# Kernel optimization log

Hardware: AMD Instinct MI355X
Metric: run time of the kernel (lower is better)

The kernel has to match this reference:

```python
import jax, jax.numpy as jnp
import numpy as np

N_NODES = 100000
N_EDGES = 1600000
D = 64
N_RELS = 200
LEAKY_SLOPE = 0.01


def setup_inputs() -> dict:
    key = jax.random.key(0)
    ks = jax.random.split(key, 12)
    def xavier(k, shape):
        gain = float(np.sqrt(2.0))  # calculate_gain('relu')
        bound = gain * float(np.sqrt(6.0 / (shape[0] + shape[1])))
        return jax.random.uniform(k, shape, jnp.float32, -bound, bound)
    return {
        "h": jax.random.normal(ks[0], (N_NODES, D), jnp.float32),
        "rel_emb": jax.random.normal(ks[1], (N_RELS, D), jnp.float32),
        "weight_neighbor": xavier(ks[2], (2 * D, D)),
        "attn_w": (xavier(ks[3], (3 * D, 1))).reshape(3 * D),
        "delta": jnp.ones((1,), jnp.float32),
        "loop_weight": xavier(ks[4], (D, D)),
        "evolve_loop_weight": xavier(ks[5], (D, D)),
        "etime": jax.random.uniform(ks[6], (N_EDGES,), jnp.float32),
        "src": jax.random.randint(ks[7], (N_EDGES,), 0, N_NODES),
        "dst": jax.random.randint(ks[8], (N_EDGES,), 0, N_NODES),
        "etype": jax.random.randint(ks[9], (N_EDGES,), 0, N_RELS),
    }


def reference(h, rel_emb, weight_neighbor, attn_w, delta, loop_weight,
              evolve_loop_weight, etime, src, dst, etype):
    N, d = h.shape
    # cat(src_h, rel) @ W  ==  src_h @ W[:d] + rel @ W[d:]  (precompute per node / per relation)
    hW = h @ weight_neighbor[:d]                 # [N, d]
    relW = rel_emb @ weight_neighbor[d:]         # [R, d]
    # attn_fc(cat(src_h, dst_h, rel)) == per-node/per-rel scalar contributions
    a1, a2, a3 = attn_w[:d], attn_w[d:2 * d], attn_w[2 * d:]
    s_src = h @ a1                               # [N]
    s_dst = h @ a2                               # [N]
    s_rel = rel_emb @ a3                         # [R]
    e = jax.nn.leaky_relu(s_src[src] + s_dst[dst] + s_rel[etype], LEAKY_SLOPE)  # [E]
    k = -etime * delta[0]                        # [E]
    scores = k * e                               # [E]
    # segment softmax over in-edges of each destination node
    m = jax.ops.segment_max(scores, dst, num_segments=N)          # [N]
    ex = jnp.exp(scores - m[dst])                                  # [E]
    den = jax.ops.segment_sum(ex, dst, num_segments=N)             # [N]
    w = ex / den[dst]                                              # [E]
    msg = hW[src] + relW[etype]                                    # [E, d]
    agg = jax.ops.segment_sum(w[:, None] * msg, dst, num_segments=N)  # [N, d]
    # nodes with no in-edges keep original h (DGL update_all semantics)
    deg = jax.ops.segment_sum(jnp.ones_like(scores), dst, num_segments=N)
    has_in = (deg > 0)[:, None]
    loop = jnp.where(has_in, h @ loop_weight, h @ evolve_loop_weight)
    node_repr = jnp.where(has_in, agg, h) + loop
    return node_repr
```

## Files before the change

kernel.cpp:

```cpp
#include <hip/hip_runtime.h>
#include <hip/hip_bf16.h>

#define N_NODES 100000
#define N_EDGES 1600000
#define D       64
#define N_RELS  200
#define LEAKY   0.01f
#define NBUCK   ((N_NODES + 511) / 512)
#define BIN_CHUNK 4096
#define NBIN    ((N_EDGES + BIN_CHUNK - 1) / BIN_CHUNK)

typedef __hip_bfloat16 bf16;

__device__ __forceinline__ float b2f(bf16 x) { return __bfloat162float(x); }
__device__ __forceinline__ bf16  f2b(float x) { return __float2bfloat16(x); }

__device__ __forceinline__ float ldf(const void* p, long i, int bf) {
    return bf ? __bfloat162float(((const bf16*)p)[i]) : ((const float*)p)[i];
}
__device__ __forceinline__ int probe_bf(const void* delta) {
    return ((const unsigned short*)delta)[0] == 0x3F80 ? 1 : 0;
}

__device__ __forceinline__ int rl_i(int v, int l) {
    return __builtin_amdgcn_readlane(v, l);
}
__device__ __forceinline__ float rl_f(float v, int l) {
    return __int_as_float(__builtin_amdgcn_readlane(__float_as_int(v), l));
}

__global__ __launch_bounds__(512, 4) void k_fused_proj(const void* __restrict__ h,
                                                       const void* __restrict__ wn,
                                                       const void* __restrict__ attn,
                                                       const void* __restrict__ delta,
                                                       const void* __restrict__ rel_emb,
                                                       const int* __restrict__ dst,
                                                       bf16* __restrict__ hWb,
                                                       float* __restrict__ s_src,
                                                       float* __restrict__ s_dst,
                                                       float* __restrict__ relW,
                                                       float* __restrict__ s_rel,
                                                       int* __restrict__ bcnt) {
    __shared__ int bh[NBUCK];
    const int bf = probe_bf(delta);
    const int wave = threadIdx.x >> 6;
    const int lane = threadIdx.x & 63;
    const int gw = blockIdx.x * 8 + wave;
    const int nwaves = gridDim.x * 8;
    float wreg[D];
    #pragma unroll
    for (int k = 0; k < D; k++) wreg[k] = ldf(wn, (long)k * D + lane, bf);
    const float a1 = ldf(attn, lane, bf);
    const float a2 = ldf(attn, D + lane, bf);
    for (int base = gw * 4; base < N_NODES; base += nwaves * 4) {
        float hv[4], acc[4];
        #pragma unroll
        for (int j = 0; j < 4; j++) {
            hv[j] = ldf(h, (long)(base + j) * D + lane, bf);
            acc[j] = 0.f;
        }
        #pragma unroll
        for (int j = 0; j < 4; j++) {
            float p1 = hv[j] * a1, p2 = hv[j] * a2;
            #pragma unroll
            for (int off = 32; off; off >>= 1) { p1 += __shfl_xor(p1, off); p2 += __shfl_xor(p2, off); }
            if (lane == 0) { s_src[base + j] = p1; s_dst[base + j] = p2; }
        }
        #pragma unroll
        for (int k = 0; k < D; k++) {
            float w = wreg[k];
            acc[0] += rl_f(hv[0], k) * w;
            acc[1] += rl_f(hv[1], k) * w;
            acc[2] += rl_f(hv[2], k) * w;
            acc[3] += rl_f(hv[3], k) * w;
        }
        #pragma unroll
        for (int j = 0; j < 4; j++) hWb[(long)(base + j) * D + lane] = f2b(acc[j]);
    }
    const float a3 = ldf(attn, 2 * D + lane, bf);
    for (int r = gw; r < N_RELS; r += nwaves) {
        float rv = ldf(rel_emb, (long)r * D + lane, bf);
        float p3 = rv * a3;
        #pragma unroll
        for (int off = 32; off; off >>= 1) p3 += __shfl_xor(p3, off);
        if (lane == 0) s_rel[r] = p3;
        float acc = 0.f;
        #pragma unroll
        for (int k = 0; k < D; k++) {
            acc += rl_f(rv, k) * ldf(wn, (long)(D + k) * D + lane, bf);
        }
        relW[r * D + lane] = acc;
    }
    for (int t = threadIdx.x; t < NBUCK; t += 512) bh[t] = 0;
    __syncthreads();
    for (int t = blockIdx.x * 512 + threadIdx.x; t < N_EDGES; t += gridDim.x * 512)
        atomicAdd(&bh[dst[t] >> 9], 1);
    __syncthreads();
    for (int t = threadIdx.x; t < NBUCK; t += 512) {
        int v = bh[t];
        if (v) atomicAdd(&bcnt[t], v);
    }
}

__global__ __launch_bounds__(256) void k_bscan(const int* __restrict__ bcnt,
                                               int* __restrict__ bbase,
                                               int* __restrict__ bcursor,
                                               int* __restrict__ rowptr) {
    __shared__ int s[256];
    const int tid = threadIdx.x;
    int v = (tid < NBUCK) ? bcnt[tid] : 0;
    s[tid] = v;
    __syncthreads();
    for (int off = 1; off < 256; off <<= 1) {
        int t = (tid >= off) ? s[tid - off] : 0;
        __syncthreads();
        s[tid] += t;
        __syncthreads();
    }
    if (tid < NBUCK) {
        int e = s[tid] - v;
        bbase[tid] = e;
        bcursor[tid] = e;
    }
    if (tid == 255) {
        bbase[NBUCK] = s[255];
        rowptr[N_NODES] = s[255];
    }
}

__global__ __launch_bounds__(512, 2) void k_bin(const float* __restrict__ s_src,
                                                const float* __restrict__ s_dst,
                                                const float* __restrict__ s_rel,
                                                const void* __restrict__ etime,
                                                const void* __restrict__ delta,
                                                const int* __restrict__ src,
                                                const int* __restrict__ dst,
                                                const int* __restrict__ etype,
                                                int* __restrict__ bcursor,
                                                int4* __restrict__ binned) {
    __shared__ int lh[NBUCK];
    __shared__ int lbase[NBUCK];
    __shared__ int gbase[NBUCK];
    __shared__ int sc[256];
    __shared__ int4 stage[BIN_CHUNK];
    const int bf = probe_bf(delta);
    const float df = ldf(delta, 0, bf);
    const int tid = threadIdx.x;
    const int base = blockIdx.x * BIN_CHUNK;
    for (int t = tid; t < NBUCK; t += 512) lh[t] = 0;
    __syncthreads();
    int4 rc[8];
    int rk[8], bk[8];
    #pragma unroll
    for (int j = 0; j < 8; j++) {
        int e = base + j * 512 + tid;
        bk[j] = -1;
        if (e < N_EDGES) {
            int s = src[e], d = dst[e], r = etype[e];
            float scv = s_src[s] + s_dst[d] + s_rel[r];
            float lre = scv > 0.f ? scv : LEAKY * scv;
            float score = (-ldf(etime, e, bf) * df) * lre;
            rc[j].x = __float_as_int(__expf(score));
            rc[j].y = s | (r << 17);
            rc[j].z = d & 511;
            rc[j].w = 0;
            int b = d >> 9;
            bk[j] = b;
            rk[j] = atomicAdd(&lh[b], 1);
        }
    }
    __syncthreads();
    if (tid < 256) sc[tid] = (tid < NBUCK) ? lh[tid] : 0;
    __syncthreads();
    for (int off = 1; off < 256; off <<= 1) {
        int t = 0;
        if (tid < 256 && tid >= off) t = sc[tid - off];
        __syncthreads();
        if (tid < 256) sc[tid] += t;
        __syncthreads();
    }
    if (tid < NBUCK) {
        lbase[tid] = sc[tid] - lh[tid];
        if (lh[tid] > 0) gbase[tid] = atomicAdd(&bcursor[tid], lh[tid]);
    }
    __syncthreads();
    #pragma unroll
    for (int j = 0; j < 8; j++) {
        if (bk[j] >= 0) stage[lbase[bk[j]] + rk[j]] = rc[j];
    }
    __syncthreads();
    const int wave = tid >> 6, lane = tid & 63;
    for (int b = wave; b < NBUCK; b += 8) {
        int n = lh[b];
        if (!n) continue;
        int ls = lbase[b];
        int gd = gbase[b];
        for (int k = lane; k < n; k += 64) binned[gd + k] = stage[ls + k];
    }
}

__global__ __launch_bounds__(1024) void k_bucket(const int4* __restrict__ binned,
                                                 const int* __restrict__ bbase,
                                                 int* __restrict__ rowptr,
                                                 int2* __restrict__ sorted) {
    __shared__ int fh[512];
    __shared__ int fc[512];
    __shared__ int sc[512];
    const int tid = threadIdx.x;
    const int b = blockIdx.x;
    const int n0 = b << 9;
    const int s0 = bbase[b], s1 = bbase[b + 1];
    if (tid < 512) { fh[tid] = 0; fc[tid] = 0; }
    __syncthreads();
    for (int i = s0 + tid; i < s1; i += 1024) atomicAdd(&fh[binned[i].z], 1);
    __syncthreads();
    if (tid < 512) sc[tid] = fh[tid];
    __syncthreads();
    for (int off = 1; off < 512; off <<= 1) {
        int t = 0;
        if (tid < 512 && tid >= off) t = sc[tid - off];
        __syncthreads();
        if (tid < 512) sc[tid] += t;
        __syncthreads();
    }
    int excl = 0;
    if (tid < 512) excl = sc[tid] - fh[tid];
    __syncthreads();
    if (tid < 512) {
        fh[tid] = excl;
        if (n0 + tid < N_NODES) rowptr[n0 + tid] = s0 + excl;
    }
    __syncthreads();
    for (int i = s0 + tid; i < s1; i += 1024) {
        int4 r = binned[i];
        int p = s0 + fh[r.z] + atomicAdd(&fc[r.z], 1);
        sorted[p] = make_int2(r.x, r.y);
    }
}

__global__ __launch_bounds__(512, 4) void k_loop(const void* __restrict__ h,
                                                 const void* __restrict__ loopW,
                                                 const void* __restrict__ delta,
                                                 float* __restrict__ L) {
    const int bf = probe_bf(delta);
    const int wave = threadIdx.x >> 6;
    const int lane = threadIdx.x & 63;
    const int gw = blockIdx.x * 8 + wave;
    const int nwaves = gridDim.x * 8;
    float wreg[D];
    #pragma unroll
    for (int k = 0; k < D; k++) wreg[k] = ldf(loopW, (long)k * D + lane, bf);
    for (int base = gw * 4; base < N_NODES; base += nwaves * 4) {
        float hv[4], acc[4];
        #pragma unroll
        for (int j = 0; j < 4; j++) {
            hv[j] = ldf(h, (long)(base + j) * D + lane, bf);
            acc[j] = 0.f;
        }
        #pragma unroll
        for (int k = 0; k < D; k++) {
            float w = wreg[k];
            acc[0] += rl_f(hv[0], k) * w;
            acc[1] += rl_f(hv[1], k) * w;
            acc[2] += rl_f(hv[2], k) * w;
            acc[3] += rl_f(hv[3], k) * w;
        }
        #pragma unroll
        for (int j = 0; j < 4; j++) L[(long)(base + j) * D + lane] = acc[j];
    }
}

__global__ __launch_bounds__(512, 8) void k_aggregate(const int* __restrict__ rowptr,
                                                      const int2* __restrict__ sorted,
                                                      const bf16* __restrict__ hWb,
                                                      const float* __restrict__ relW,
                                                      const void* __restrict__ h,
                                                      const void* __restrict__ evolveW,
                                                      const float* __restrict__ L,
                                                      const void* __restrict__ delta,
                                                      float* __restrict__ out) {
    const int bf = probe_bf(delta);
    const int wave = threadIdx.x >> 6;
    const int lane = threadIdx.x & 63;
    const int grp  = lane >> 4;
    const int sub  = lane & 15;
    const unsigned sub8  = (unsigned)sub << 3;
    const unsigned sub16 = (unsigned)sub << 4;
    const int wstride = gridDim.x * 8;
    for (int i = blockIdx.x * 8 + wave; i < N_NODES; i += wstride) {
        const int s0 = rowptr[i], e1 = rowptr[i + 1];
        if (e1 > s0) {
            float ax = 0.f, ay = 0.f, az = 0.f, aw = 0.f;
            float ls = 0.f;
            for (int c = s0; c < e1; c += 64) {
                int n = e1 - c; n = n > 64 ? 64 : n;
                float exl = 0.f; int pk = 0;
                if (lane < n) {
                    int2 rec = sorted[c + lane];
                    exl = __int_as_float(rec.x);
                    pk = rec.y;
                }
                float cs = exl;
                #pragma unroll
                for (int off = 32; off; off >>= 1) cs += __shfl_xor(cs, off);
                ls += cs;
                #pragma unroll 2
                for (int j = 0; j < n; j += 4) {
                    float w = __shfl(exl, j + grp);
                    int   p = __shfl(pk,  j + grp);
                    unsigned hoff = ((unsigned)(p & 0x1FFFF) << 7) + sub8;
                    unsigned roff = ((unsigned)(p >> 17) << 8) + sub16;
                    uint2  hw = *(const uint2*) ((const char*)hWb  + hoff);
                    float4 rw = *(const float4*)((const char*)relW + roff);
                    float f0 = __uint_as_float(hw.x << 16);
                    float f1 = __uint_as_float(hw.x & 0xFFFF0000u);
                    float f2 = __uint_as_float(hw.y << 16);
                    float f3 = __uint_as_float(hw.y & 0xFFFF0000u);
                    ax += w * (f0 + rw.x);
                    ay += w * (f1 + rw.y);
                    az += w * (f2 + rw.z);
                    aw += w * (f3 + rw.w);
                }
            }
            ax += __shfl_xor(ax, 16); ax += __shfl_xor(ax, 32);
            ay += __shfl_xor(ay, 16); ay += __shfl_xor(ay, 32);
            az += __shfl_xor(az, 16); az += __shfl_xor(az, 32);
            aw += __shfl_xor(aw, 16); aw += __shfl_xor(aw, 32);
            if (grp == 0) {
                const float inv = 1.f / ls;
                const float4 l4 = *(const float4*)(L + (long)i * D + sub * 4);
                float4 r;
                r.x = ax * inv + l4.x;
                r.y = ay * inv + l4.y;
                r.z = az * inv + l4.z;
                r.w = aw * inv + l4.w;
                *(float4*)(out + (long)i * D + sub * 4) = r;
            }
        } else {
            float hv = ldf(h, (long)i * D + lane, bf);
            float acc = hv;
            for (int k = 0; k < D; k++)
                acc += rl_f(hv, k) * ldf(evolveW, (long)k * D + lane, bf);
            out[(long)i * D + lane] = acc;
        }
    }
}

__global__ __launch_bounds__(256) void k_fallback(float* __restrict__ out) {
    int t = blockIdx.x * blockDim.x + threadIdx.x;
    if (t < N_NODES * D) out[t] = 0.f;
}

extern "C" void kernel_launch(void* const* d_in, const int* in_sizes, int n_in,
                              void* d_out, int out_size, void* d_ws, size_t ws_size,
                              hipStream_t stream) {
    const void* h       = d_in[0];
    const void* rel_emb = d_in[1];
    const void* wn      = d_in[2];
    const void* attn    = d_in[3];
    const void* delta   = d_in[4];
    const void* loopW   = d_in[5];
    const void* evolveW = d_in[6];
    const void* etime   = d_in[7];
    const int*  src     = (const int*)d_in[8];
    const int*  dst     = (const int*)d_in[9];
    const int*  etype   = (const int*)d_in[10];
    float* out = (float*)d_out;

    char* ws = (char*)d_ws;
    size_t off = 0;
    auto alloc = [&](size_t bytes) -> void* {
        off = (off + 255) & ~(size_t)255;
        void* p = ws + off;
        off += bytes;
        return p;
    };
    int4*  binned  = (int4*) alloc((size_t)N_EDGES * 16);
    int2*  sorted  = (int2*) alloc((size_t)N_EDGES * 8);
    bf16*  hWb     = (bf16*) alloc((size_t)N_NODES * D * 2);
    float* relW    = (float*)alloc((size_t)N_RELS * D * 4);
    float* s_src   = (float*)alloc((size_t)N_NODES * 4);
    float* s_dst   = (float*)alloc((size_t)N_NODES * 4);
    float* s_rel   = (float*)alloc((size_t)N_RELS * 4);
    int*   rowptr  = (int*)  alloc((size_t)(N_NODES + 1) * 4);
    int*   bcnt    = (int*)  alloc((size_t)NBUCK * 4);
    int*   bbase   = (int*)  alloc((size_t)(NBUCK + 1) * 4);
    int*   bcursor = (int*)  alloc((size_t)NBUCK * 4);

    float* L = (float*)binned;

    if (ws_size < off) {
        k_fallback<<<(N_NODES * D + 255) / 256, 256, 0, stream>>>(out);
        return;
    }

    hipMemsetAsync(bcnt, 0, (size_t)NBUCK * 4, stream);
    k_fused_proj<<<1024, 512, 0, stream>>>(h, wn, attn, delta, rel_emb, dst,
                                           hWb, s_src, s_dst, relW, s_rel, bcnt);
    k_bscan<<<1, 256, 0, stream>>>(bcnt, bbase, bcursor, rowptr);
    k_bin<<<NBIN, 512, 0, stream>>>(s_src, s_dst, s_rel, etime, delta,
                                    src, dst, etype, bcursor, binned);
    k_bucket<<<NBUCK, 1024, 0, stream>>>(binned, bbase, rowptr, sorted);
    k_loop<<<1024, 512, 0, stream>>>(h, loopW, delta, L);
    k_aggregate<<<2048, 512, 0, stream>>>(rowptr, sorted, hWb, relW, h, evolveW, L, delta, out);
}
```

Measured before the change: 309.7 us.

## Shrink binned edge records, use finer buckets, drop LDS staging in binning

The binned edge record drops from 16 bytes to an 8-byte payload plus a separate byte-sized local index, and buckets shrink from 512 to 256 nodes, so the bucket sort handles smaller groups. k_bin no longer stages records in shared memory and instead scatters directly to global positions, which removes an LDS scan and a copy pass but makes the writes less coalesced. The projection kernel now processes 8 nodes per wave instead of 4, runs with a smaller grid, and only 256 blocks build the histogram. Launch bounds are raised to 8 blocks per CU, which may cause register spills in the 64-register weight loops.

```diff
diff --git a/kernel.cpp b/kernel.cpp
--- a/kernel.cpp
+++ b/kernel.cpp
@@ -6,9 +6,11 @@
 #define D       64
 #define N_RELS  200
 #define LEAKY   0.01f
-#define NBUCK   ((N_NODES + 511) / 512)
-#define BIN_CHUNK 4096
-#define NBIN    ((N_EDGES + BIN_CHUNK - 1) / BIN_CHUNK)
+#define NBUCK      391
+#define BUCK_SHIFT 8
+#define BUCK_MASK  255
+#define BIN_CHUNK  4096
+#define NBIN       ((N_EDGES + BIN_CHUNK - 1) / BIN_CHUNK)
 
 typedef __hip_bfloat16 bf16;
 
@@ -29,7 +31,7 @@
     return __int_as_float(__builtin_amdgcn_readlane(__float_as_int(v), l));
 }
 
-__global__ __launch_bounds__(512, 4) void k_fused_proj(const void* __restrict__ h,
+__global__ __launch_bounds__(512, 8) void k_fused_proj(const void* __restrict__ h,
                                                        const void* __restrict__ wn,
                                                        const void* __restrict__ attn,
                                                        const void* __restrict__ delta,
@@ -52,15 +54,15 @@
     for (int k = 0; k < D; k++) wreg[k] = ldf(wn, (long)k * D + lane, bf);
     const float a1 = ldf(attn, lane, bf);
     const float a2 = ldf(attn, D + lane, bf);
-    for (int base = gw * 4; base < N_NODES; base += nwaves * 4) {
-        float hv[4], acc[4];
-        #pragma unroll
-        for (int j = 0; j < 4; j++) {
+    for (int base = gw * 8; base < N_NODES; base += nwaves * 8) {
+        float hv[8], acc[8];
+        #pragma unroll
+        for (int j = 0; j < 8; j++) {
             hv[j] = ldf(h, (long)(base + j) * D + lane, bf);
             acc[j] = 0.f;
         }
         #pragma unroll
-        for (int j = 0; j < 4; j++) {
+        for (int j = 0; j < 8; j++) {
             float p1 = hv[j] * a1, p2 = hv[j] * a2;
             #pragma unroll
             for (int off = 32; off; off >>= 1) { p1 += __shfl_xor(p1, off); p2 += __shfl_xor(p2, off); }
@@ -69,13 +71,11 @@
         #pragma unroll
         for (int k = 0; k < D; k++) {
             float w = wreg[k];
-            acc[0] += rl_f(hv[0], k) * w;
-            acc[1] += rl_f(hv[1], k) * w;
-            acc[2] += rl_f(hv[2], k) * w;
-            acc[3] += rl_f(hv[3], k) * w;
-        }
-        #pragma unroll
-        for (int j = 0; j < 4; j++) hWb[(long)(base + j) * D + lane] = f2b(acc[j]);
+            #pragma unroll
+            for (int j = 0; j < 8; j++) acc[j] += rl_f(hv[j], k) * w;
+        }
+        #pragma unroll
+        for (int j = 0; j < 8; j++) hWb[(long)(base + j) * D + lane] = f2b(acc[j]);
     }
     const float a3 = ldf(attn, 2 * D + lane, bf);
     for (int r = gw; r < N_RELS; r += nwaves) {
@@ -91,27 +91,29 @@
         }
         relW[r * D + lane] = acc;
     }
-    for (int t = threadIdx.x; t < NBUCK; t += 512) bh[t] = 0;
-    __syncthreads();
-    for (int t = blockIdx.x * 512 + threadIdx.x; t < N_EDGES; t += gridDim.x * 512)
-        atomicAdd(&bh[dst[t] >> 9], 1);
-    __syncthreads();
-    for (int t = threadIdx.x; t < NBUCK; t += 512) {
-        int v = bh[t];
-        if (v) atomicAdd(&bcnt[t], v);
-    }
-}
-
-__global__ __launch_bounds__(256) void k_bscan(const int* __restrict__ bcnt,
+    if (blockIdx.x < 256) {
+        for (int t = threadIdx.x; t < NBUCK; t += 512) bh[t] = 0;
+        __syncthreads();
+        for (int t = blockIdx.x * 512 + threadIdx.x; t < N_EDGES; t += 256 * 512)
+            atomicAdd(&bh[dst[t] >> BUCK_SHIFT], 1);
+        __syncthreads();
+        for (int t = threadIdx.x; t < NBUCK; t += 512) {
+            int v = bh[t];
+            if (v) atomicAdd(&bcnt[t], v);
+        }
+    }
+}
+
+__global__ __launch_bounds__(512) void k_bscan(const int* __restrict__ bcnt,
                                                int* __restrict__ bbase,
                                                int* __restrict__ bcursor,
                                                int* __restrict__ rowptr) {
-    __shared__ int s[256];
+    __shared__ int s[512];
     const int tid = threadIdx.x;
     int v = (tid < NBUCK) ? bcnt[tid] : 0;
     s[tid] = v;
     __syncthreads();
-    for (int off = 1; off < 256; off <<= 1) {
+    for (int off = 1; off < 512; off <<= 1) {
         int t = (tid >= off) ? s[tid - off] : 0;
         __syncthreads();
         s[tid] += t;
@@ -122,13 +124,13 @@
         bbase[tid] = e;
         bcursor[tid] = e;
     }
-    if (tid == 255) {
-        bbase[NBUCK] = s[255];
-        rowptr[N_NODES] = s[255];
-    }
-}
-
-__global__ __launch_bounds__(512, 2) void k_bin(const float* __restrict__ s_src,
+    if (tid == 511) {
+        bbase[NBUCK] = s[511];
+        rowptr[N_NODES] = s[511];
+    }
+}
+
+__global__ __launch_bounds__(512, 8) void k_bin(const float* __restrict__ s_src,
                                                 const float* __restrict__ s_dst,
                                                 const float* __restrict__ s_rel,
                                                 const void* __restrict__ etime,
@@ -137,20 +139,18 @@
                                                 const int* __restrict__ dst,
                                                 const int* __restrict__ etype,
                                                 int* __restrict__ bcursor,
-                                                int4* __restrict__ binned) {
+                                                int2* __restrict__ payl,
+                                                unsigned char* __restrict__ zbuf) {
     __shared__ int lh[NBUCK];
-    __shared__ int lbase[NBUCK];
     __shared__ int gbase[NBUCK];
-    __shared__ int sc[256];
-    __shared__ int4 stage[BIN_CHUNK];
     const int bf = probe_bf(delta);
     const float df = ldf(delta, 0, bf);
     const int tid = threadIdx.x;
     const int base = blockIdx.x * BIN_CHUNK;
     for (int t = tid; t < NBUCK; t += 512) lh[t] = 0;
     __syncthreads();
-    int4 rc[8];
-    int rk[8], bk[8];
+    int2 rc[8];
+    int rk[8], bk[8], zz[8];
     #pragma unroll
     for (int j = 0; j < 8; j++) {
         int e = base + j * 512 + tid;
@@ -162,15 +162,45 @@
             float score = (-ldf(etime, e, bf) * df) * lre;
             rc[j].x = __float_as_int(__expf(score));
             rc[j].y = s | (r << 17);
-            rc[j].z = d & 511;
-            rc[j].w = 0;
-            int b = d >> 9;
+            zz[j] = d & BUCK_MASK;
+            int b = d >> BUCK_SHIFT;
             bk[j] = b;
             rk[j] = atomicAdd(&lh[b], 1);
         }
     }
     __syncthreads();
-    if (tid < 256) sc[tid] = (tid < NBUCK) ? lh[tid] : 0;
+    for (int t = tid; t < NBUCK; t += 512) {
+        int v = lh[t];
+        if (v) gbase[t] = atomicAdd(&bcursor[t], v);
+    }
+    __syncthreads();
+    #pragma unroll
+    for (int j = 0; j < 8; j++) {
+        if (bk[j] >= 0) {
+            int pos = gbase[bk[j]] + rk[j];
+            payl[pos] = rc[j];
+            zbuf[pos] = (unsigned char)zz[j];
+        }
+    }
+}
+
+__global__ __launch_bounds__(512) void k_bucket(const int2* __restrict__ payl,
+                                                const unsigned char* __restrict__ zbuf,
+                                                const int* __restrict__ bbase,
+                                                int* __restrict__ rowptr,
+                                                int2* __restrict__ sorted) {
+    __shared__ int fh[256];
+    __shared__ int fc[256];
+    __shared__ int sc[256];
+    const int tid = threadIdx.x;
+    const int b = blockIdx.x;
+    const int n0 = b << BUCK_SHIFT;
+    const int s0 = bbase[b], s1 = bbase[b + 1];
+    if (tid < 256) { fh[tid] = 0; fc[tid] = 0; }
+    __syncthreads();
+    for (int i = s0 + tid; i < s1; i += 512) atomicAdd(&fh[zbuf[i]], 1);
+    __syncthreads();
+    if (tid < 256) sc[tid] = fh[tid];
     __syncthreads();
     for (int off = 1; off < 256; off <<= 1) {
         int t = 0;
@@ -179,66 +209,21 @@
         if (tid < 256) sc[tid] += t;
         __syncthreads();
     }
-    if (tid < NBUCK) {
-        lbase[tid] = sc[tid] - lh[tid];
-        if (lh[tid] > 0) gbase[tid] = atomicAdd(&bcursor[tid], lh[tid]);
-    }
-    __syncthreads();
-    #pragma unroll
-    for (int j = 0; j < 8; j++) {
-        if (bk[j] >= 0) stage[lbase[bk[j]] + rk[j]] = rc[j];
-    }
-    __syncthreads();
-    const int wave = tid >> 6, lane = tid & 63;
-    for (int b = wave; b < NBUCK; b += 8) {
-        int n = lh[b];
-        if (!n) continue;
-        int ls = lbase[b];
-        int gd = gbase[b];
-        for (int k = lane; k < n; k += 64) binned[gd + k] = stage[ls + k];
-    }
-}
-
-__global__ __launch_bounds__(1024) void k_bucket(const int4* __restrict__ binned,
-                                                 const int* __restrict__ bbase,
-                                                 int* __restrict__ rowptr,
-                                                 int2* __restrict__ sorted) {
-    __shared__ int fh[512];
-    __shared__ int fc[512];
-    __shared__ int sc[512];
-    const int tid = threadIdx.x;
-    const int b = blockIdx.x;
-    const int n0 = b << 9;
-    const int s0 = bbase[b], s1 = bbase[b + 1];
-    if (tid < 512) { fh[tid] = 0; fc[tid] = 0; }
-    __syncthreads();
-    for (int i = s0 + tid; i < s1; i += 1024) atomicAdd(&fh[binned[i].z], 1);
-    __syncthreads();
-    if (tid < 512) sc[tid] = fh[tid];
-    __syncthreads();
-    for (int off = 1; off < 512; off <<= 1) {
-        int t = 0;
-        if (tid < 512 && tid >= off) t = sc[tid - off];
-        __syncthreads();
-        if (tid < 512) sc[tid] += t;
-        __syncthreads();
-    }
-    int excl = 0;
-    if (tid < 512) excl = sc[tid] - fh[tid];
-    __syncthreads();
-    if (tid < 512) {
+    if (tid < 256) {
+        int excl = sc[tid] - fh[tid];
         fh[tid] = excl;
         if (n0 + tid < N_NODES) rowptr[n0 + tid] = s0 + excl;
     }
     __syncthreads();
-    for (int i = s0 + tid; i < s1; i += 1024) {
-        int4 r = binned[i];
-        int p = s0 + fh[r.z] + atomicAdd(&fc[r.z], 1);
-        sorted[p] = make_int2(r.x, r.y);
-    }
-}
-
-__global__ __launch_bounds__(512, 4) void k_loop(const void* __restrict__ h,
+    for (int i = s0 + tid; i < s1; i += 512) {
+        int2 r = payl[i];
+        int z = zbuf[i];
+        int p = s0 + fh[z] + atomicAdd(&fc[z], 1);
+        sorted[p] = r;
+    }
+}
+
+__global__ __launch_bounds__(512, 8) void k_loop(const void* __restrict__ h,
                                                  const void* __restrict__ loopW,
                                                  const void* __restrict__ delta,
                                                  float* __restrict__ L) {
@@ -375,7 +360,7 @@
         off += bytes;
         return p;
     };
-    int4*  binned  = (int4*) alloc((size_t)N_EDGES * 16);
+    char*  regionA = (char*) alloc((size_t)N_NODES * D * 4);
     int2*  sorted  = (int2*) alloc((size_t)N_EDGES * 8);
     bf16*  hWb     = (bf16*) alloc((size_t)N_NODES * D * 2);
     float* relW    = (float*)alloc((size_t)N_RELS * D * 4);
@@ -387,7 +372,9 @@
     int*   bbase   = (int*)  alloc((size_t)(NBUCK + 1) * 4);
     int*   bcursor = (int*)  alloc((size_t)NBUCK * 4);
 
-    float* L = (float*)binned;
+    int2* payl = (int2*)regionA;
+    unsigned char* zbuf = (unsigned char*)(regionA + (size_t)N_EDGES * 8);
+    float* L = (float*)regionA;
 
     if (ws_size < off) {
         k_fallback<<<(N_NODES * D + 255) / 256, 256, 0, stream>>>(out);
@@ -395,12 +382,12 @@
     }
 
     hipMemsetAsync(bcnt, 0, (size_t)NBUCK * 4, stream);
-    k_fused_proj<<<1024, 512, 0, stream>>>(h, wn, attn, delta, rel_emb, dst,
-                                           hWb, s_src, s_dst, relW, s_rel, bcnt);
-    k_bscan<<<1, 256, 0, stream>>>(bcnt, bbase, bcursor, rowptr);
+    k_fused_proj<<<781, 512, 0, stream>>>(h, wn, attn, delta, rel_emb, dst,
+                                          hWb, s_src, s_dst, relW, s_rel, bcnt);
+    k_bscan<<<1, 512, 0, stream>>>(bcnt, bbase, bcursor, rowptr);
     k_bin<<<NBIN, 512, 0, stream>>>(s_src, s_dst, s_rel, etime, delta,
-                                    src, dst, etype, bcursor, binned);
-    k_bucket<<<NBUCK, 1024, 0, stream>>>(binned, bbase, rowptr, sorted);
-    k_loop<<<1024, 512, 0, stream>>>(h, loopW, delta, L);
+                                    src, dst, etype, bcursor, payl, zbuf);
+    k_bucket<<<NBUCK, 512, 0, stream>>>(payl, zbuf, bbase, rowptr, sorted);
+    k_loop<<<781, 512, 0, stream>>>(h, loopW, delta, L);
     k_aggregate<<<2048, 512, 0, stream>>>(rowptr, sorted, hWb, relW, h, evolveW, L, delta, out);
 }
```

Result: slower. 719.7 us (+132.4%).
